# Optimization experiments

Measured on AMD Instinct MI355X. Metric: run time of the kernel, lower is better.

Reference implementation:

```python
import jax, jax.numpy as jnp
import numpy as np

N_USER = 80000
N_ITEM = 20000
N = N_USER + N_ITEM          # total nodes
E = 1600000                  # edges (nnz of norm_adj), avg degree 16
EMB = 64                     # emb_size
FEAT = 64                    # feature_dim -> input_dim = 128
D = EMB + FEAT               # 128
L = 3                        # number of GCN layers, layer_size=[128,128,128]
K = 3                        # max_hop
B = 4096                     # batch_size


def setup_inputs() -> dict:
    key = jax.random.key(0)
    ks = jax.random.split(key, 16)
    deg_scale = 1.0 / 16.0  # ~normalized adjacency values
    return {
        'edge_row': jax.random.randint(ks[0], (E,), 0, N, dtype=jnp.int32),
        'edge_col': jax.random.randint(ks[1], (E,), 0, N, dtype=jnp.int32),
        'edge_val': jax.random.uniform(ks[2], (E,), dtype=jnp.float32) * deg_scale,
        'feat': jax.random.normal(ks[3], (N_USER, FEAT), dtype=jnp.float32) * 0.1,
        'user_emb': jax.random.normal(ks[4], (N_USER, EMB), dtype=jnp.float32) * 0.1,
        'item_emb1': jax.random.normal(ks[5], (N_ITEM, EMB), dtype=jnp.float32) * 0.1,
        'item_emb2': jax.random.normal(ks[6], (N_ITEM, FEAT), dtype=jnp.float32) * 0.1,
        'alphas': jax.random.normal(ks[7], (L, K), dtype=jnp.float32) * 0.1,
        'W_gc': jax.random.normal(ks[8], (L, D, D), dtype=jnp.float32) * 0.05,
        'b_gc': jax.random.normal(ks[9], (L, 1, D), dtype=jnp.float32) * 0.05,
        'W_bi': jax.random.normal(ks[10], (L, D, D), dtype=jnp.float32) * 0.05,
        'b_bi': jax.random.normal(ks[11], (L, 1, D), dtype=jnp.float32) * 0.05,
        'users': jax.random.randint(ks[12], (B,), 0, N_USER, dtype=jnp.int32),
        'pos_items': jax.random.randint(ks[13], (B,), 0, N_ITEM, dtype=jnp.int32),
        'neg_items': jax.random.randint(ks[14], (B,), 0, N_ITEM, dtype=jnp.int32),
    }


def reference(edge_row, edge_col, edge_val, feat, user_emb, item_emb1,
              item_emb2, alphas, W_gc, b_gc, W_bi, b_bi,
              users, pos_items, neg_items):
    def spmm(X):
        # A_hat @ X via edge-list gather + segment-sum (sparse.mm equivalent)
        return jax.ops.segment_sum(edge_val[:, None] * X[edge_col], edge_row,
                                   num_segments=N)

    # ego embeddings: [[user_emb|feat], [item_emb1|item_emb2]] -> [N, D]
    ego = jnp.concatenate([
        jnp.concatenate([user_emb, item_emb1], axis=0),
        jnp.concatenate([feat, item_emb2], axis=0),
    ], axis=1)

    all_embs = [ego]
    for k in range(L):
        # multi-order aggregation: sum_i beta_i * A^i @ ego
        beta = jax.nn.softmax(alphas[k])
        cur = spmm(ego)
        side = beta[0] * cur
        for i in range(1, K):
            cur = spmm(cur)
            side = side + beta[i] * cur
        sum_e = side @ W_gc[k] + b_gc[k]
        bi_e = (ego * side) @ W_bi[k] + b_bi[k]
        # aggregator_mode == 'sum_bi'
        ego = jax.nn.leaky_relu(sum_e, negative_slope=0.2) + bi_e
        # mess_dropout = 0 -> identity; L2-normalize rows (F.normalize eps=1e-12)
        norm = ego / jnp.maximum(
            jnp.linalg.norm(ego, axis=1, keepdims=True), 1e-12)
        all_embs.append(norm)

    all_emb = jnp.concatenate(all_embs, axis=1)  # [N, D*(L+1)] = [N, 512]
    u_emb = all_emb[:N_USER]
    i_emb = all_emb[N_USER:]
    return (u_emb[users], i_emb[pos_items], i_emb[neg_items])
```

## Files before the change

kernel.cpp:

```cpp
#include <hip/hip_runtime.h>
#include <hip/hip_bf16.h>

typedef __hip_bfloat16 hbf16;
typedef unsigned short u16;
typedef __bf16 bf16x8 __attribute__((ext_vector_type(8)));
typedef float f32x4 __attribute__((ext_vector_type(4)));

#define N_USERS 80000
#define N_ITEMS 20000
#define NTOT    100000
#define NEDGE   1600000
#define DDIM    128
#define NLAY    3
#define KHOP    3
#define NB      4096
#define LBM     128
#define NBUK    98
#define BROWS   1024
#define BSH     10

__device__ inline u16 f2bfu(float f) { __bf16 h = (__bf16)f; return __builtin_bit_cast(u16, h); }

__global__ void build_ego_kernel(const float* __restrict__ feat, const float* __restrict__ user_emb,
                                 const float* __restrict__ item_emb1, const float* __restrict__ item_emb2,
                                 u16* __restrict__ ego, int* __restrict__ bbins) {
    if (blockIdx.x == 0 && threadIdx.x < NBUK) bbins[threadIdx.x] = 0;
    int i = blockIdx.x * 256 + threadIdx.x;
    int n = i >> 7, d = i & 127;
    float v;
    if (n < N_USERS) {
        v = (d < 64) ? user_emb[n*64 + d] : feat[n*64 + d - 64];
    } else {
        int m = n - N_USERS;
        v = (d < 64) ? item_emb1[m*64 + d] : item_emb2[m*64 + d - 64];
    }
    ego[i] = f2bfu(v);
}

__global__ void transpose_w_kernel(const float* __restrict__ Wgc, const float* __restrict__ Wbi,
                                   u16* __restrict__ WTgc, u16* __restrict__ WTbi) {
    __shared__ float t[32][33];
    int z = blockIdx.z;
    const float* W = (z < 3) ? (Wgc + (size_t)z * 16384) : (Wbi + (size_t)(z - 3) * 16384);
    u16* WT = (z < 3) ? (WTgc + (size_t)z * 16384) : (WTbi + (size_t)(z - 3) * 16384);
    int r0 = blockIdx.y * 32, c0 = blockIdx.x * 32;
    for (int i = threadIdx.y; i < 32; i += 8)
        t[i][threadIdx.x] = W[(size_t)(r0 + i) * 128 + c0 + threadIdx.x];
    __syncthreads();
    for (int i = threadIdx.y; i < 32; i += 8)
        WT[(size_t)(c0 + i) * 128 + r0 + threadIdx.x] = f2bfu(t[threadIdx.x][i]);
}

__global__ __launch_bounds__(256) void bhist_kernel(const int* __restrict__ er,
                                                    int* __restrict__ bbins) {
    __shared__ int l[NBUK];
    int tid = threadIdx.x;
    if (tid < NBUK) l[tid] = 0;
    __syncthreads();
    for (int i = blockIdx.x * 256 + tid; i < NEDGE; i += gridDim.x * 256)
        atomicAdd(&l[er[i] >> BSH], 1);
    __syncthreads();
    if (tid < NBUK && l[tid]) atomicAdd(&bbins[tid], l[tid]);
}

__global__ void beta_bscan_kernel(const float* __restrict__ alphas, float* __restrict__ beta,
                                  const int* __restrict__ bbins, int* __restrict__ bbase,
                                  int* __restrict__ bcur) {
    if (threadIdx.x == 0 && blockIdx.x == 0) {
        for (int k = 0; k < NLAY; ++k) {
            float a[KHOP];
            float m = -1e30f;
            for (int i = 0; i < KHOP; ++i) { a[i] = alphas[k*KHOP+i]; m = fmaxf(m, a[i]); }
            float s = 0.f;
            for (int i = 0; i < KHOP; ++i) { a[i] = expf(a[i] - m); s += a[i]; }
            for (int i = 0; i < KHOP; ++i) beta[k*KHOP+i] = a[i] / s;
        }
        int acc = 0;
        for (int b = 0; b < NBUK; ++b) { int t = bbins[b]; bbase[b] = acc; bcur[b] = acc; acc += t; }
        bbase[NBUK] = acc;
    }
}

__global__ __launch_bounds__(256) void bappend_kernel(
    const int* __restrict__ er, const int* __restrict__ ec, const float* __restrict__ ev,
    int* __restrict__ bcur, int* __restrict__ tmprow, int2* __restrict__ tmpcv) {
    __shared__ int lcnt[NBUK], lbase[NBUK], lrank[NBUK];
    int tid = threadIdx.x;
    for (int b = tid; b < NBUK; b += 256) { lcnt[b] = 0; lrank[b] = 0; }
    __syncthreads();
    int base = blockIdx.x * 2048;
    int r[8], c[8], vb[8], bk[8];
    bool ok[8];
    #pragma unroll
    for (int k = 0; k < 8; ++k) {
        int i = base + k * 256 + tid;
        ok[k] = i < NEDGE;
        bk[k] = 0;
        if (ok[k]) {
            r[k] = er[i]; c[k] = ec[i]; vb[k] = __float_as_int(ev[i]);
            bk[k] = r[k] >> BSH;
            atomicAdd(&lcnt[bk[k]], 1);
        }
    }
    __syncthreads();
    for (int b = tid; b < NBUK; b += 256)
        lbase[b] = lcnt[b] ? atomicAdd(&bcur[b], lcnt[b]) : 0;
    __syncthreads();
    #pragma unroll
    for (int k = 0; k < 8; ++k) {
        if (ok[k]) {
            int rank = atomicAdd(&lrank[bk[k]], 1);
            int pos = lbase[bk[k]] + rank;
            tmprow[pos] = r[k];
            tmpcv[pos] = make_int2(c[k], vb[k]);
        }
    }
}

__global__ __launch_bounds__(1024) void bfinal_kernel(
    const int* __restrict__ bbase, const int* __restrict__ tmprow,
    const int2* __restrict__ tmpcv, int* __restrict__ rowptr, int2* __restrict__ edges) {
    __shared__ int lhist[BROWS];
    __shared__ int s2[1024];
    int b = blockIdx.x, tid = threadIdx.x;
    int s = bbase[b], e = bbase[b + 1];
    int rbase = b << BSH;
    int nrows = min(NTOT - rbase, BROWS);
    lhist[tid] = 0;
    __syncthreads();
    for (int i = s + tid; i < e; i += 1024)
        atomicAdd(&lhist[tmprow[i] - rbase], 1);
    __syncthreads();
    int a = lhist[tid];
    s2[tid] = a;
    __syncthreads();
    for (int off = 1; off < 1024; off <<= 1) {
        int t = (tid >= off) ? s2[tid - off] : 0;
        __syncthreads();
        s2[tid] += t;
        __syncthreads();
    }
    int excl = s2[tid] - a;
    if (tid < nrows) rowptr[rbase + tid] = s + excl;
    if (b == NBUK - 1 && tid == 0) rowptr[NTOT] = NEDGE;
    lhist[tid] = excl;
    __syncthreads();
    for (int i = s + tid; i < e; i += 1024) {
        int lr = tmprow[i] - rbase;
        int p = atomicAdd(&lhist[lr], 1);
        edges[s + p] = tmpcv[i];
    }
}

__device__ inline void ld_edge_nt(const int2* __restrict__ p, int& c, float& v) {
    unsigned long long rec =
        __builtin_nontemporal_load(reinterpret_cast<const unsigned long long*>(p));
    c = (int)(unsigned)(rec & 0xffffffffull);
    v = __int_as_float((int)(unsigned)(rec >> 32));
}

__global__ __launch_bounds__(256) void spmm_kernel(
    const int* __restrict__ rowptr, const int2* __restrict__ edges,
    const u16* __restrict__ X, u16* __restrict__ Y) {
    int tid = threadIdx.x;
    int r = blockIdx.x * 16 + (tid >> 4);
    int lane = tid & 15;
    int s = rowptr[r], e = rowptr[r + 1];
    float acc[8];
    #pragma unroll
    for (int i = 0; i < 8; ++i) acc[i] = 0.f;
    const u16* xb = X + lane * 8;
    int j = s;
    for (; j + 8 <= e; j += 8) {
        int cc[8]; float vv[8];
        #pragma unroll
        for (int u = 0; u < 8; ++u) ld_edge_nt(edges + j + u, cc[u], vv[u]);
        bf16x8 x[8];
        #pragma unroll
        for (int u = 0; u < 8; ++u)
            x[u] = *reinterpret_cast<const bf16x8*>(xb + (size_t)cc[u] * DDIM);
        __builtin_amdgcn_sched_barrier(0);
        #pragma unroll
        for (int u = 0; u < 8; ++u) {
            #pragma unroll
            for (int i = 0; i < 8; ++i) acc[i] = fmaf(vv[u], (float)x[u][i], acc[i]);
        }
    }
    for (; j + 4 <= e; j += 4) {
        int cc[4]; float vv[4];
        #pragma unroll
        for (int u = 0; u < 4; ++u) ld_edge_nt(edges + j + u, cc[u], vv[u]);
        bf16x8 x[4];
        #pragma unroll
        for (int u = 0; u < 4; ++u)
            x[u] = *reinterpret_cast<const bf16x8*>(xb + (size_t)cc[u] * DDIM);
        __builtin_amdgcn_sched_barrier(0);
        #pragma unroll
        for (int u = 0; u < 4; ++u) {
            #pragma unroll
            for (int i = 0; i < 8; ++i) acc[i] = fmaf(vv[u], (float)x[u][i], acc[i]);
        }
    }
    for (; j < e; ++j) {
        int cc; float vv;
        ld_edge_nt(edges + j, cc, vv);
        bf16x8 x = *reinterpret_cast<const bf16x8*>(xb + (size_t)cc * DDIM);
        #pragma unroll
        for (int i = 0; i < 8; ++i) acc[i] = fmaf(vv, (float)x[i], acc[i]);
    }
    size_t oi = (size_t)r * DDIM + lane * 8;
    bf16x8 y;
    #pragma unroll
    for (int i = 0; i < 8; ++i) y[i] = (__bf16)acc[i];
    *reinterpret_cast<bf16x8*>(Y + oi) = y;
}

__global__ __launch_bounds__(512, 4) void layer_kernel(
    const u16* __restrict__ ego, const u16* __restrict__ h1,
    const u16* __restrict__ h2, const u16* __restrict__ h3,
    const float* __restrict__ beta3,
    const u16* __restrict__ wtgc, const u16* __restrict__ wtbi,
    const float* __restrict__ bgc, const float* __restrict__ bbi,
    u16* __restrict__ ego_out, u16* __restrict__ normbuf) {
    __shared__ __align__(16) unsigned char smem[65536];
    const int WG = 0, WB = 32768;
    int tid = threadIdx.x;
    int base = blockIdx.x * LBM;
    float b0 = beta3[0], b1 = beta3[1], b2 = beta3[2];

    #pragma unroll
    for (int p = 0; p < 4; ++p) {
        int slot = tid + p * 512;
        int n = slot >> 4, ks = slot & 15;
        uint4 g  = *reinterpret_cast<const uint4*>(wtgc + n * DDIM + ks * 8);
        uint4 bq = *reinterpret_cast<const uint4*>(wtbi + n * DDIM + ks * 8);
        int addr = n * 256 + ((ks * 16) ^ ((n & 7) << 4));
        *reinterpret_cast<uint4*>(&smem[WG + addr]) = g;
        *reinterpret_cast<uint4*>(&smem[WB + addr]) = bq;
    }
    __syncthreads();

    int l = tid & 63, w = tid >> 6;
    int m = l & 15, g16 = l >> 4;
    int sw = (m & 7) << 4;
    int grow = base + w * 16 + m;
    bool ok = grow < NTOT;
    int grc = ok ? grow : 0;
    size_t aoff = (size_t)grc * DDIM + g16 * 8;

    bf16x8 c1 = *reinterpret_cast<const bf16x8*>(h1 + aoff);
    bf16x8 c2 = *reinterpret_cast<const bf16x8*>(h2 + aoff);
    bf16x8 c3 = *reinterpret_cast<const bf16x8*>(h3 + aoff);
    bf16x8 ce = *reinterpret_cast<const bf16x8*>(ego + aoff);

    f32x4 accg[8], accb[8];
    #pragma unroll
    for (int nt = 0; nt < 8; ++nt) {
        accg[nt] = (f32x4){0.f, 0.f, 0.f, 0.f};
        accb[nt] = (f32x4){0.f, 0.f, 0.f, 0.f};
    }
    #pragma unroll
    for (int kk = 0; kk < 4; ++kk) {
        bf16x8 p1, p2, p3, pe;
        if (kk < 3) {
            p1 = *reinterpret_cast<const bf16x8*>(h1 + aoff + (kk + 1) * 32);
            p2 = *reinterpret_cast<const bf16x8*>(h2 + aoff + (kk + 1) * 32);
            p3 = *reinterpret_cast<const bf16x8*>(h3 + aoff + (kk + 1) * 32);
            pe = *reinterpret_cast<const bf16x8*>(ego + aoff + (kk + 1) * 32);
            __builtin_amdgcn_sched_barrier(0);
        }
        bf16x8 as, ab;
        #pragma unroll
        for (int i = 0; i < 8; ++i) {
            float sf = ok ? (b0 * (float)c1[i] + b1 * (float)c2[i] + b2 * (float)c3[i]) : 0.f;
            as[i] = (__bf16)sf;
            ab[i] = (__bf16)(sf * (float)ce[i]);
        }
        int ka = (kk * 64 + g16 * 16) ^ sw;
        #pragma unroll
        for (int nt = 0; nt < 8; ++nt) {
            int na = (nt * 16 + m) * 256 + ka;
            bf16x8 bg = *reinterpret_cast<const bf16x8*>(&smem[WG + na]);
            accg[nt] = __builtin_amdgcn_mfma_f32_16x16x32_bf16(as, bg, accg[nt], 0, 0, 0);
            bf16x8 bb = *reinterpret_cast<const bf16x8*>(&smem[WB + na]);
            accb[nt] = __builtin_amdgcn_mfma_f32_16x16x32_bf16(ab, bb, accb[nt], 0, 0, 0);
        }
        if (kk < 3) { c1 = p1; c2 = p2; c3 = p3; ce = pe; }
    }
    float bgv[8], bbv[8];
    #pragma unroll
    for (int nt = 0; nt < 8; ++nt) { bgv[nt] = bgc[nt * 16 + m]; bbv[nt] = bbi[nt * 16 + m]; }
    float ss[4] = {0.f, 0.f, 0.f, 0.f};
    #pragma unroll
    for (int nt = 0; nt < 8; ++nt) {
        #pragma unroll
        for (int rr = 0; rr < 4; ++rr) {
            float se = accg[nt][rr] + bgv[nt];
            float be = accb[nt][rr] + bbv[nt];
            float v = (se > 0.f ? se : 0.2f * se) + be;
            accg[nt][rr] = v;
            ss[rr] += v * v;
            int row = base + w * 16 + g16 * 4 + rr;
            if (row < NTOT) ego_out[(size_t)row * DDIM + nt * 16 + m] = f2bfu(v);
        }
    }
    #pragma unroll
    for (int rr = 0; rr < 4; ++rr) {
        ss[rr] += __shfl_xor(ss[rr], 1, 64);
        ss[rr] += __shfl_xor(ss[rr], 2, 64);
        ss[rr] += __shfl_xor(ss[rr], 4, 64);
        ss[rr] += __shfl_xor(ss[rr], 8, 64);
        ss[rr] = 1.f / fmaxf(sqrtf(ss[rr]), 1e-12f);
    }
    #pragma unroll
    for (int nt = 0; nt < 8; ++nt) {
        #pragma unroll
        for (int rr = 0; rr < 4; ++rr) {
            int row = base + w * 16 + g16 * 4 + rr;
            if (row < NTOT) normbuf[(size_t)row * DDIM + nt * 16 + m] = f2bfu(accg[nt][rr] * ss[rr]);
        }
    }
}

__global__ void gather_ego_kernel(const float* __restrict__ feat, const float* __restrict__ user_emb,
                                  const float* __restrict__ item_emb1, const float* __restrict__ item_emb2,
                                  const int* __restrict__ users, const int* __restrict__ pos,
                                  const int* __restrict__ neg, float* __restrict__ out) {
    int i = blockIdx.x * 256 + threadIdx.x;
    int which = i / (NB * DDIM);
    int rem = i - which * (NB * DDIM);
    int b = rem >> 7, d = rem & 127;
    float v;
    if (which == 0) {
        int u = users[b];
        v = (d < 64) ? user_emb[u*64 + d] : feat[u*64 + d - 64];
    } else {
        int m = (which == 1) ? pos[b] : neg[b];
        v = (d < 64) ? item_emb1[m*64 + d] : item_emb2[m*64 + d - 64];
    }
    out[(size_t)which * NB * 512 + (size_t)b * 512 + d] = v;
}

__global__ void gather_slice_kernel(const u16* __restrict__ src, const int* __restrict__ users,
                                    const int* __restrict__ pos, const int* __restrict__ neg,
                                    float* __restrict__ out, int slot) {
    int i = blockIdx.x * 256 + threadIdx.x;
    int which = i / (NB * DDIM);
    int rem = i - which * (NB * DDIM);
    int b = rem >> 7, c = rem & 127;
    int row;
    if (which == 0)      row = users[b];
    else if (which == 1) row = N_USERS + pos[b];
    else                 row = N_USERS + neg[b];
    unsigned int u = src[(size_t)row * DDIM + c];
    out[(size_t)which * NB * 512 + (size_t)b * 512 + slot * 128 + c] =
        __builtin_bit_cast(float, u << 16);
}

extern "C" void kernel_launch(void* const* d_in, const int* in_sizes, int n_in,
                              void* d_out, int out_size, void* d_ws, size_t ws_size,
                              hipStream_t stream) {
    (void)in_sizes; (void)n_in; (void)out_size; (void)ws_size;
    const int*   edge_row  = (const int*)  d_in[0];
    const int*   edge_col  = (const int*)  d_in[1];
    const float* edge_val  = (const float*)d_in[2];
    const float* feat      = (const float*)d_in[3];
    const float* user_emb  = (const float*)d_in[4];
    const float* item_emb1 = (const float*)d_in[5];
    const float* item_emb2 = (const float*)d_in[6];
    const float* alphas    = (const float*)d_in[7];
    const float* W_gc      = (const float*)d_in[8];
    const float* b_gc      = (const float*)d_in[9];
    const float* W_bi      = (const float*)d_in[10];
    const float* b_bi      = (const float*)d_in[11];
    const int*   users     = (const int*)  d_in[12];
    const int*   pos_items = (const int*)  d_in[13];
    const int*   neg_items = (const int*)  d_in[14];
    float* out = (float*)d_out;

    char* ws = (char*)d_ws;
    size_t off = 0;
    auto alloc = [&](size_t bytes) -> char* {
        char* p = ws + off;
        off = (off + bytes + 255) & ~(size_t)255;
        return p;
    };
    u16*   ego      = (u16*)  alloc((size_t)NTOT * DDIM * 2);
    u16*   h1       = (u16*)  alloc((size_t)NTOT * DDIM * 2);
    u16*   h2       = (u16*)  alloc((size_t)NTOT * DDIM * 2);
    u16*   h3       = (u16*)  alloc((size_t)NTOT * DDIM * 2);
    u16*   normbuf  = (u16*)  alloc((size_t)NTOT * DDIM * 2);
    int*   rowptr   = (int*)  alloc((size_t)(NTOT + 1) * 4);
    int*   bbins    = (int*)  alloc((NBUK + 2) * 4);
    int*   bbase    = (int*)  alloc((NBUK + 2) * 4);
    int*   bcur     = (int*)  alloc((NBUK + 2) * 4);
    int2*  edges    = (int2*) alloc((size_t)NEDGE * 8);
    u16*   wtgc     = (u16*)  alloc((size_t)NLAY * DDIM * DDIM * 2);
    u16*   wtbi     = (u16*)  alloc((size_t)NLAY * DDIM * DDIM * 2);
    float* beta     = (float*)alloc(256);

    int*  tmprow = (int*)h1;
    int2* tmpcv  = (int2*)((char*)h1 + (size_t)NEDGE * 4);

    build_ego_kernel<<<(NTOT * DDIM) / 256, 256, 0, stream>>>(feat, user_emb, item_emb1, item_emb2,
                                                              ego, bbins);
    transpose_w_kernel<<<dim3(4, 4, 6), dim3(32, 8), 0, stream>>>(W_gc, W_bi, wtgc, wtbi);

    bhist_kernel<<<256, 256, 0, stream>>>(edge_row, bbins);
    beta_bscan_kernel<<<1, 64, 0, stream>>>(alphas, beta, bbins, bbase, bcur);
    bappend_kernel<<<(NEDGE + 2047) / 2048, 256, 0, stream>>>(edge_row, edge_col, edge_val,
                                                              bcur, tmprow, tmpcv);
    bfinal_kernel<<<NBUK, 1024, 0, stream>>>(bbase, tmprow, tmpcv, rowptr, edges);

    gather_ego_kernel<<<(3 * NB * DDIM) / 256, 256, 0, stream>>>(feat, user_emb, item_emb1, item_emb2,
                                                                 users, pos_items, neg_items, out);

    int lgrid = (NTOT + LBM - 1) / LBM;
    for (int k = 0; k < NLAY; ++k) {
        spmm_kernel<<<NTOT / 16, 256, 0, stream>>>(rowptr, edges, ego, h1);
        spmm_kernel<<<NTOT / 16, 256, 0, stream>>>(rowptr, edges, h1, h2);
        spmm_kernel<<<NTOT / 16, 256, 0, stream>>>(rowptr, edges, h2, h3);
        layer_kernel<<<lgrid, 512, 0, stream>>>(ego, h1, h2, h3, beta + 3 * k,
                                                wtgc + (size_t)k * DDIM * DDIM, wtbi + (size_t)k * DDIM * DDIM,
                                                b_gc + (size_t)k * DDIM, b_bi + (size_t)k * DDIM,
                                                ego, normbuf);
        gather_slice_kernel<<<(3 * NB * DDIM) / 256, 256, 0, stream>>>(normbuf, users, pos_items, neg_items, out, k + 1);
    }
}
```

Baseline: 801.9 us.

## Split edge arrays with bf16 values and write normalized rows only for batch nodes

Edge storage changes from interleaved int2 (column, fp32 value) to separate int32 column and bf16 value arrays. This cuts the edge stream bytes read by each of the nine SpMM passes from 8 to 6 per edge. The layer kernel also writes the normalized output rows only for nodes flagged as referenced by users/pos/neg, which removes most of the normbuf write traffic. The costs are lower precision on the adjacency weights and a per-row flag load in the layer epilogue.

```diff
diff --git a/kernel.cpp b/kernel.cpp
--- a/kernel.cpp
+++ b/kernel.cpp
@@ -20,13 +20,16 @@
 #define BSH     10
 
 __device__ inline u16 f2bfu(float f) { __bf16 h = (__bf16)f; return __builtin_bit_cast(u16, h); }
+__device__ inline float bfu2f(u16 u) { return __builtin_bit_cast(float, (unsigned)u << 16); }
 
 __global__ void build_ego_kernel(const float* __restrict__ feat, const float* __restrict__ user_emb,
                                  const float* __restrict__ item_emb1, const float* __restrict__ item_emb2,
-                                 u16* __restrict__ ego, int* __restrict__ bbins) {
+                                 u16* __restrict__ ego, int* __restrict__ bbins,
+                                 unsigned char* __restrict__ flags) {
     if (blockIdx.x == 0 && threadIdx.x < NBUK) bbins[threadIdx.x] = 0;
     int i = blockIdx.x * 256 + threadIdx.x;
     int n = i >> 7, d = i & 127;
+    if (d == 0) flags[n] = 0;
     float v;
     if (n < N_USERS) {
         v = (d < 64) ? user_emb[n*64 + d] : feat[n*64 + d - 64];
@@ -119,7 +122,8 @@
 
 __global__ __launch_bounds__(1024) void bfinal_kernel(
     const int* __restrict__ bbase, const int* __restrict__ tmprow,
-    const int2* __restrict__ tmpcv, int* __restrict__ rowptr, int2* __restrict__ edges) {
+    const int2* __restrict__ tmpcv, int* __restrict__ rowptr,
+    int* __restrict__ ecol, u16* __restrict__ eval) {
     __shared__ int lhist[BROWS];
     __shared__ int s2[1024];
     int b = blockIdx.x, tid = threadIdx.x;
@@ -146,21 +150,17 @@
     lhist[tid] = excl;
     __syncthreads();
     for (int i = s + tid; i < e; i += 1024) {
+        int2 rec = tmpcv[i];
         int lr = tmprow[i] - rbase;
         int p = atomicAdd(&lhist[lr], 1);
-        edges[s + p] = tmpcv[i];
-    }
-}
-
-__device__ inline void ld_edge_nt(const int2* __restrict__ p, int& c, float& v) {
-    unsigned long long rec =
-        __builtin_nontemporal_load(reinterpret_cast<const unsigned long long*>(p));
-    c = (int)(unsigned)(rec & 0xffffffffull);
-    v = __int_as_float((int)(unsigned)(rec >> 32));
+        ecol[s + p] = rec.x;
+        eval[s + p] = f2bfu(__int_as_float(rec.y));
+    }
 }
 
 __global__ __launch_bounds__(256) void spmm_kernel(
-    const int* __restrict__ rowptr, const int2* __restrict__ edges,
+    const int* __restrict__ rowptr, const int* __restrict__ ecol,
+    const u16* __restrict__ eval,
     const u16* __restrict__ X, u16* __restrict__ Y) {
     int tid = threadIdx.x;
     int r = blockIdx.x * 16 + (tid >> 4);
@@ -174,7 +174,9 @@
     for (; j + 8 <= e; j += 8) {
         int cc[8]; float vv[8];
         #pragma unroll
-        for (int u = 0; u < 8; ++u) ld_edge_nt(edges + j + u, cc[u], vv[u]);
+        for (int u = 0; u < 8; ++u) cc[u] = __builtin_nontemporal_load(ecol + j + u);
+        #pragma unroll
+        for (int u = 0; u < 8; ++u) vv[u] = bfu2f(__builtin_nontemporal_load(eval + j + u));
         bf16x8 x[8];
         #pragma unroll
         for (int u = 0; u < 8; ++u)
@@ -189,7 +191,9 @@
     for (; j + 4 <= e; j += 4) {
         int cc[4]; float vv[4];
         #pragma unroll
-        for (int u = 0; u < 4; ++u) ld_edge_nt(edges + j + u, cc[u], vv[u]);
+        for (int u = 0; u < 4; ++u) cc[u] = __builtin_nontemporal_load(ecol + j + u);
+        #pragma unroll
+        for (int u = 0; u < 4; ++u) vv[u] = bfu2f(__builtin_nontemporal_load(eval + j + u));
         bf16x8 x[4];
         #pragma unroll
         for (int u = 0; u < 4; ++u)
@@ -202,8 +206,8 @@
         }
     }
     for (; j < e; ++j) {
-        int cc; float vv;
-        ld_edge_nt(edges + j, cc, vv);
+        int cc = __builtin_nontemporal_load(ecol + j);
+        float vv = bfu2f(__builtin_nontemporal_load(eval + j));
         bf16x8 x = *reinterpret_cast<const bf16x8*>(xb + (size_t)cc * DDIM);
         #pragma unroll
         for (int i = 0; i < 8; ++i) acc[i] = fmaf(vv, (float)x[i], acc[i]);
@@ -221,6 +225,7 @@
     const float* __restrict__ beta3,
     const u16* __restrict__ wtgc, const u16* __restrict__ wtbi,
     const float* __restrict__ bgc, const float* __restrict__ bbi,
+    const unsigned char* __restrict__ flags,
     u16* __restrict__ ego_out, u16* __restrict__ normbuf) {
     __shared__ __align__(16) unsigned char smem[65536];
     const int WG = 0, WB = 32768;
@@ -312,12 +317,14 @@
         ss[rr] += __shfl_xor(ss[rr], 8, 64);
         ss[rr] = 1.f / fmaxf(sqrtf(ss[rr]), 1e-12f);
     }
-    #pragma unroll
-    for (int nt = 0; nt < 8; ++nt) {
-        #pragma unroll
-        for (int rr = 0; rr < 4; ++rr) {
-            int row = base + w * 16 + g16 * 4 + rr;
-            if (row < NTOT) normbuf[(size_t)row * DDIM + nt * 16 + m] = f2bfu(accg[nt][rr] * ss[rr]);
+    int frow = base + w * 16 + g16 * 4;
+    #pragma unroll
+    for (int rr = 0; rr < 4; ++rr) {
+        int row = frow + rr;
+        if (row < NTOT && flags[row]) {
+            #pragma unroll
+            for (int nt = 0; nt < 8; ++nt)
+                normbuf[(size_t)row * DDIM + nt * 16 + m] = f2bfu(accg[nt][rr] * ss[rr]);
         }
     }
 }
@@ -325,19 +332,24 @@
 __global__ void gather_ego_kernel(const float* __restrict__ feat, const float* __restrict__ user_emb,
                                   const float* __restrict__ item_emb1, const float* __restrict__ item_emb2,
                                   const int* __restrict__ users, const int* __restrict__ pos,
-                                  const int* __restrict__ neg, float* __restrict__ out) {
+                                  const int* __restrict__ neg, float* __restrict__ out,
+                                  unsigned char* __restrict__ flags) {
     int i = blockIdx.x * 256 + threadIdx.x;
     int which = i / (NB * DDIM);
     int rem = i - which * (NB * DDIM);
     int b = rem >> 7, d = rem & 127;
     float v;
+    int row;
     if (which == 0) {
         int u = users[b];
+        row = u;
         v = (d < 64) ? user_emb[u*64 + d] : feat[u*64 + d - 64];
     } else {
         int m = (which == 1) ? pos[b] : neg[b];
+        row = N_USERS + m;
         v = (d < 64) ? item_emb1[m*64 + d] : item_emb2[m*64 + d - 64];
     }
+    if (d == 0) flags[row] = 1;
     out[(size_t)which * NB * 512 + (size_t)b * 512 + d] = v;
 }
 
@@ -394,7 +406,9 @@
     int*   bbins    = (int*)  alloc((NBUK + 2) * 4);
     int*   bbase    = (int*)  alloc((NBUK + 2) * 4);
     int*   bcur     = (int*)  alloc((NBUK + 2) * 4);
-    int2*  edges    = (int2*) alloc((size_t)NEDGE * 8);
+    int*   ecol     = (int*)  alloc((size_t)NEDGE * 4);
+    u16*   eval     = (u16*)  alloc((size_t)NEDGE * 2);
+    unsigned char* flags = (unsigned char*)alloc(NTOT + 512);
     u16*   wtgc     = (u16*)  alloc((size_t)NLAY * DDIM * DDIM * 2);
     u16*   wtbi     = (u16*)  alloc((size_t)NLAY * DDIM * DDIM * 2);
     float* beta     = (float*)alloc(256);
@@ -403,27 +417,27 @@
     int2* tmpcv  = (int2*)((char*)h1 + (size_t)NEDGE * 4);
 
     build_ego_kernel<<<(NTOT * DDIM) / 256, 256, 0, stream>>>(feat, user_emb, item_emb1, item_emb2,
-                                                              ego, bbins);
+                                                              ego, bbins, flags);
     transpose_w_kernel<<<dim3(4, 4, 6), dim3(32, 8), 0, stream>>>(W_gc, W_bi, wtgc, wtbi);
 
     bhist_kernel<<<256, 256, 0, stream>>>(edge_row, bbins);
     beta_bscan_kernel<<<1, 64, 0, stream>>>(alphas, beta, bbins, bbase, bcur);
     bappend_kernel<<<(NEDGE + 2047) / 2048, 256, 0, stream>>>(edge_row, edge_col, edge_val,
                                                               bcur, tmprow, tmpcv);
-    bfinal_kernel<<<NBUK, 1024, 0, stream>>>(bbase, tmprow, tmpcv, rowptr, edges);
+    bfinal_kernel<<<NBUK, 1024, 0, stream>>>(bbase, tmprow, tmpcv, rowptr, ecol, eval);
 
     gather_ego_kernel<<<(3 * NB * DDIM) / 256, 256, 0, stream>>>(feat, user_emb, item_emb1, item_emb2,
-                                                                 users, pos_items, neg_items, out);
+                                                                 users, pos_items, neg_items, out, flags);
 
     int lgrid = (NTOT + LBM - 1) / LBM;
     for (int k = 0; k < NLAY; ++k) {
-        spmm_kernel<<<NTOT / 16, 256, 0, stream>>>(rowptr, edges, ego, h1);
-        spmm_kernel<<<NTOT / 16, 256, 0, stream>>>(rowptr, edges, h1, h2);
-        spmm_kernel<<<NTOT / 16, 256, 0, stream>>>(rowptr, edges, h2, h3);
+        spmm_kernel<<<NTOT / 16, 256, 0, stream>>>(rowptr, ecol, eval, ego, h1);
+        spmm_kernel<<<NTOT / 16, 256, 0, stream>>>(rowptr, ecol, eval, h1, h2);
+        spmm_kernel<<<NTOT / 16, 256, 0, stream>>>(rowptr, ecol, eval, h2, h3);
         layer_kernel<<<lgrid, 512, 0, stream>>>(ego, h1, h2, h3, beta + 3 * k,
                                                 wtgc + (size_t)k * DDIM * DDIM, wtbi + (size_t)k * DDIM * DDIM,
                                                 b_gc + (size_t)k * DDIM, b_bi + (size_t)k * DDIM,
-                                                ego, normbuf);
+                                                flags, ego, normbuf);
         gather_slice_kernel<<<(3 * NB * DDIM) / 256, 256, 0, stream>>>(normbuf, users, pos_items, neg_items, out, k + 1);
     }
 }
```

Measured after the change: 838.9 us. +4.6%, slower.
